# Performance work log

Hardware: AMD Instinct MI355X
Metric: run time of the kernel (lower is better)

The kernel has to match this reference:

```python
import jax, jax.numpy as jnp
import numpy as np

D_MODEL = 768
N_HEAD = 12
D_HEAD = D_MODEL // N_HEAD
B, T = 2, 2048


def setup_inputs() -> dict:
    key = jax.random.key(0)
    k1, k2, k3 = jax.random.split(key, 3)
    x = jax.random.normal(k1, (B, T, D_MODEL), dtype=jnp.float32)
    w_attn = jax.random.normal(k2, (D_MODEL, 3 * D_MODEL), dtype=jnp.float32) * (1.0 / np.sqrt(D_MODEL))
    b_attn = jnp.zeros((3 * D_MODEL,), dtype=jnp.float32)
    w_proj = jax.random.normal(k3, (D_MODEL, D_MODEL), dtype=jnp.float32) * (1.0 / np.sqrt(D_MODEL))
    b_proj = jnp.zeros((D_MODEL,), dtype=jnp.float32)
    return {"x": x, "w_attn": w_attn, "b_attn": b_attn, "w_proj": w_proj, "b_proj": b_proj}


def reference(x, w_attn, b_attn, w_proj, b_proj):
    Bq, Tq, C = x.shape
    qkv = x @ w_attn + b_attn                                  # [B, T, 3C]
    qkv = qkv.reshape(Bq, Tq, 3, N_HEAD, D_HEAD)
    q, k, v = qkv[:, :, 0], qkv[:, :, 1], qkv[:, :, 2]         # [B, T, H, Dh]
    scale = 1.0 / np.sqrt(D_HEAD)
    att = jnp.einsum('bqhd,bkhd->bhqk', q, k) * scale          # [B, H, T, T]
    causal = jnp.tril(jnp.ones((Tq, Tq), dtype=bool))
    att = jnp.where(causal[None, None], att, -jnp.inf)
    att = jax.nn.softmax(att, axis=-1)
    y = jnp.einsum('bhqk,bkhd->bqhd', att, v).reshape(Bq, Tq, C)
    return y @ w_proj + b_proj
```

## Files before the change

### kernel.cpp

```cpp
#include <hip/hip_runtime.h>
#include <hip/hip_bf16.h>

#define D_MODEL 768
#define N_HEADS 12
#define D_HEADK 64
#define BB 2
#define TT 2048
#define M_TOK (BB*TT)
#define N_QKV (3*D_MODEL)
#define MS_SEG (BB*N_HEADS*TT)

using f32x4  = __attribute__((ext_vector_type(4))) float;
using f32x16 = __attribute__((ext_vector_type(16))) float;
using s16x8  = __attribute__((ext_vector_type(8))) short;

typedef __attribute__((address_space(1))) const unsigned int ga_u32;
typedef __attribute__((address_space(3))) unsigned int ls_u32;

__device__ __forceinline__ float fast_exp2(float x) {
    return __builtin_amdgcn_exp2f(x);
}

__device__ __forceinline__ unsigned short f2bf(float f) {
    union { float f; unsigned u; } v; v.f = f;
    unsigned r = v.u + 0x7FFFu + ((v.u >> 16) & 1u);
    return (unsigned short)(r >> 16);
}

__device__ __forceinline__ float bf2f(unsigned short u) {
    union { unsigned u; float f; } v; v.u = ((unsigned)u) << 16; return v.f;
}

__device__ __forceinline__ unsigned cvtpk_bf16(float lo, float hi) {
    unsigned d;
    asm("v_cvt_pk_bf16_f32 %0, %1, %2" : "=v"(d) : "v"(lo), "v"(hi));
    return d;
}

__global__ void xbf_kernel(const float* __restrict__ X, unsigned short* __restrict__ Xb) {
    int idx = (blockIdx.x * 256 + threadIdx.x) * 8;
    float4 v0 = *(const float4*)&X[idx];
    float4 v1 = *(const float4*)&X[idx + 4];
    ushort4 u0, u1;
    u0.x = f2bf(v0.x); u0.y = f2bf(v0.y); u0.z = f2bf(v0.z); u0.w = f2bf(v0.w);
    u1.x = f2bf(v1.x); u1.y = f2bf(v1.y); u1.z = f2bf(v1.z); u1.w = f2bf(v1.w);
    *(ushort4*)&Xb[idx]     = u0;
    *(ushort4*)&Xb[idx + 4] = u1;
}

__global__ void wtrans_kernel(const float* __restrict__ Wa, const float* __restrict__ Wp,
                              unsigned short* __restrict__ Wta, unsigned short* __restrict__ Wtp) {
    const float* W; unsigned short* Wt; int N;
    if (blockIdx.z == 0) { W = Wa; Wt = Wta; N = N_QKV; }
    else                 { W = Wp; Wt = Wtp; N = D_MODEL; }
    int bx = blockIdx.x * 32;
    if (bx >= N) return;
    int by = blockIdx.y * 32;
    __shared__ float tile[32][33];
    int tx = threadIdx.x & 31;
    int ty = threadIdx.x >> 5;
    #pragma unroll
    for (int i = ty; i < 32; i += 8)
        tile[i][tx] = W[(size_t)(by + i) * N + bx + tx];
    __syncthreads();
    #pragma unroll
    for (int i = ty; i < 32; i += 8)
        Wt[(size_t)(bx + i) * D_MODEL + by + tx] = f2bf(tile[tx][i]);
}

__launch_bounds__(256)
__global__ void qkv_kernel(const unsigned short* __restrict__ Xb, const unsigned short* __restrict__ Wt,
                           const float* __restrict__ bias,
                           unsigned short* __restrict__ Qw, unsigned short* __restrict__ Kw,
                           unsigned short* __restrict__ Vw) {
    __shared__ unsigned short As[128*64];
    __shared__ unsigned short Bs[128*64];
    const int m0 = blockIdx.y * 128;
    const int n0 = blockIdx.x * 128;
    const int tid = threadIdx.x;
    const int l  = tid & 63;
    const int w  = tid >> 6;
    const int wr = w >> 1, wc = w & 1;
    const int lr = l & 15, lk4 = l >> 4, li = (l >> 4) * 4;
    const int grw  = l >> 3;
    const int gslt = l & 7;

    f32x4 acc[4][4] = {};
    for (int kt = 0; kt < D_MODEL; kt += 64) {
        #pragma unroll
        for (int i = 0; i < 4; ++i) {
            const int row  = w*32 + i*8 + grw;
            const int gcol = (gslt ^ (row & 7)) << 3;
            __builtin_amdgcn_global_load_lds(
                (ga_u32*)&Xb[(size_t)(m0 + row) * D_MODEL + kt + gcol],
                (ls_u32*)&As[(w*32 + i*8) * 64], 16, 0, 0);
            __builtin_amdgcn_global_load_lds(
                (ga_u32*)&Wt[(size_t)(n0 + row) * D_MODEL + kt + gcol],
                (ls_u32*)&Bs[(w*32 + i*8) * 64], 16, 0, 0);
        }
        __syncthreads();
        #pragma unroll
        for (int ks = 0; ks < 2; ++ks) {
            s16x8 a[4], bf[4];
            #pragma unroll
            for (int mi = 0; mi < 4; ++mi) {
                const int row = wr*64 + mi*16 + lr;
                const int slot = (ks*4 + lk4) ^ (row & 7);
                a[mi] = *(const s16x8*)&As[row*64 + slot*8];
            }
            #pragma unroll
            for (int ni = 0; ni < 4; ++ni) {
                const int row = wc*64 + ni*16 + lr;
                const int slot = (ks*4 + lk4) ^ (row & 7);
                bf[ni] = *(const s16x8*)&Bs[row*64 + slot*8];
            }
            #pragma unroll
            for (int mi = 0; mi < 4; ++mi)
                #pragma unroll
                for (int ni = 0; ni < 4; ++ni)
                    acc[mi][ni] = __builtin_amdgcn_mfma_f32_16x16x32_bf16(a[mi], bf[ni], acc[mi][ni], 0, 0, 0);
        }
        __syncthreads();
    }
    #pragma unroll
    for (int ni = 0; ni < 4; ++ni) {
        int ng = n0 + wc*64 + ni*16 + lr;
        int mat = ng / D_MODEL;
        int hd  = ng % D_MODEL;
        int h = hd >> 6, d = hd & 63;
        float bv = bias[ng];
        #pragma unroll
        for (int mi = 0; mi < 4; ++mi) {
            #pragma unroll
            for (int i = 0; i < 4; ++i) {
                int t  = m0 + wr*64 + mi*16 + li + i;
                int b  = t >> 11, tq = t & 2047;
                float val = acc[mi][ni][i] + bv;
                size_t off = ((size_t)(b*N_HEADS + h)*TT + tq)*64 + d;
                if (mat == 0)      Qw[off] = f2bf(val * 0.18033688f);
                else if (mat == 1) Kw[off] = f2bf(val);
                else               Vw[off] = f2bf(val);
            }
        }
    }
}

__launch_bounds__(256)
__global__ void vtrans_kernel(const unsigned short* __restrict__ Vw, unsigned short* __restrict__ Vt) {
    __shared__ unsigned short tile[64][65];
    const int bh = blockIdx.y;
    const int t0 = blockIdx.x * 64;
    const int tid = threadIdx.x;
    const int srow = tid >> 3;
    const int scol = (tid & 7) * 8;
    const unsigned short* src = Vw + (size_t)bh * TT * 64;
    unsigned short* dst = Vt + (size_t)bh * 64 * TT;
    *(int4*)&tile[srow][scol]    = *(const int4*)&src[(size_t)(t0 + srow) * 64 + scol];
    *(int4*)&tile[srow+32][scol] = *(const int4*)&src[(size_t)(t0 + srow + 32) * 64 + scol];
    __syncthreads();
    s16x8 a0, a1;
    #pragma unroll
    for (int j = 0; j < 8; ++j) {
        a0[j] = (short)tile[scol + j][srow];
        a1[j] = (short)tile[scol + j][srow + 32];
    }
    *(s16x8*)&dst[(size_t)srow * TT + t0 + scol]        = a0;
    *(s16x8*)&dst[(size_t)(srow + 32) * TT + t0 + scol] = a1;
}

__device__ __forceinline__ int swz(int r, int c) { return r*64 + (c ^ ((r & 7) << 3)); }

__launch_bounds__(256)
__global__ void attn_kernel(const unsigned short* __restrict__ Q,
                            const unsigned short* __restrict__ Kk,
                            const unsigned short* __restrict__ Vt,
                            unsigned short* __restrict__ oA,
                            unsigned short* __restrict__ oB,
                            unsigned short* __restrict__ oC,
                            unsigned short* __restrict__ oD,
                            float* __restrict__ ms) {
    __shared__ unsigned short Ks[64*64];
    __shared__ unsigned short Vs[64*64];
    const int bh = blockIdx.y;
    const int px = blockIdx.x;
    const int qci = 15 - (px >> 2);
    const int seg = px & 3;
    const int q0 = qci * 128;
    const int b = bh / N_HEADS, h = bh % N_HEADS;
    const int tid = threadIdx.x;
    const int l  = tid & 63;
    const int w  = tid >> 6;
    const int lq = l & 31;
    const int hi = l >> 5;
    const int srow = tid >> 3;
    const int scol = (tid & 7) * 8;
    const int qw0 = q0 + w * 32;

    const unsigned short* Qp = Q  + (size_t)bh * TT * 64;
    const unsigned short* Kp = Kk + (size_t)bh * TT * 64;
    const unsigned short* Vp = Vt + (size_t)bh * 64 * TT;

    const int ntiles  = 2 * (qci + 1);
    const int t_begin = (seg * ntiles) >> 2;
    const int t_end   = ((seg + 1) * ntiles) >> 2;

    s16x8 qsel[4];
    {
        const unsigned short* qrow = &Qp[(size_t)(qw0 + lq) * 64];
        #pragma unroll
        for (int t = 0; t < 4; ++t) {
            s16x8 qlo = *(const s16x8*)&qrow[16*t];
            s16x8 qhi = *(const s16x8*)&qrow[16*t + 8];
            qsel[t] = hi ? qhi : qlo;
        }
    }

    float mi = -1e30f, si = 0.f;
    f32x16 o0 = {}, o1 = {};

    const int kb0 = t_begin * 64;
    int4 kp0 = *(const int4*)&Kp[(size_t)(kb0 + srow) * 64 + scol];
    int4 kp1 = *(const int4*)&Kp[(size_t)(kb0 + srow + 32) * 64 + scol];
    int4 vp0 = *(const int4*)&Vp[(size_t)srow * TT + kb0 + scol];
    int4 vp1 = *(const int4*)&Vp[(size_t)(srow + 32) * TT + kb0 + scol];

    for (int it = t_begin; it < t_end; ++it) {
        const int kt = it * 64;
        __syncthreads();
        *(int4*)&Ks[swz(srow,      scol)] = kp0;
        *(int4*)&Ks[swz(srow + 32, scol)] = kp1;
        *(int4*)&Vs[swz(srow,      scol)] = vp0;
        *(int4*)&Vs[swz(srow + 32, scol)] = vp1;
        __syncthreads();
        if (it + 1 < t_end) {
            const int k2 = kt + 64;
            kp0 = *(const int4*)&Kp[(size_t)(k2 + srow) * 64 + scol];
            kp1 = *(const int4*)&Kp[(size_t)(k2 + srow + 32) * 64 + scol];
            vp0 = *(const int4*)&Vp[(size_t)srow * TT + k2 + scol];
            vp1 = *(const int4*)&Vp[(size_t)(srow + 32) * TT + k2 + scol];
        }
        #pragma unroll
        for (int kti = 0; kti < 2; ++kti) {
            const int kk = kt + kti * 32;
            if (kk > qw0) continue;
            const bool diag = (kk == qw0);
            f32x16 s = {};
            #pragma unroll
            for (int t = 0; t < 4; ++t) {
                s16x8 a = *(const s16x8*)&Ks[swz(kti*32 + lq, 16*t + 8*hi)];
                s = __builtin_amdgcn_mfma_f32_32x32x16_bf16(a, qsel[t], s, 0, 0, 0);
            }
            if (diag) {
                #pragma unroll
                for (int r = 0; r < 16; ++r) {
                    const int kloc = (r & 3) + 8*(r >> 2) + 4*hi;
                    if (kloc > lq) s[r] = -1e30f;
                }
            }
            float lm = s[0];
            #pragma unroll
            for (int r = 1; r < 16; ++r) lm = fmaxf(lm, s[r]);
            if (!__all(lm <= mi + 11.5f)) {
                float pm = fmaxf(lm, __shfl_xor(lm, 32));
                float mn = fmaxf(mi, pm);
                float sf = fast_exp2(mi - mn);
                si *= sf;
                #pragma unroll
                for (int r = 0; r < 16; ++r) {
                    const int qloc = (r & 3) + 8*(r >> 2) + 4*hi;
                    float sfq = __shfl(sf, qloc);
                    o0[r] *= sfq; o1[r] *= sfq;
                }
                mi = mn;
            }
            float e[16];
            float psum = 0.f;
            #pragma unroll
            for (int r = 0; r < 16; ++r) {
                e[r] = fast_exp2(s[r] - mi);
                psum += e[r];
            }
            si += psum;
            #pragma unroll
            for (int s2 = 0; s2 < 2; ++s2) {
                unsigned c0 = cvtpk_bf16(e[8*s2 + 0], e[8*s2 + 1]);
                unsigned c1 = cvtpk_bf16(e[8*s2 + 2], e[8*s2 + 3]);
                unsigned c2 = cvtpk_bf16(e[8*s2 + 4], e[8*s2 + 5]);
                unsigned c3 = cvtpk_bf16(e[8*s2 + 6], e[8*s2 + 7]);
                asm("v_permlane32_swap_b32 %0, %1" : "+v"(c0), "+v"(c2));
                asm("v_permlane32_swap_b32 %0, %1" : "+v"(c1), "+v"(c3));
                union { unsigned u[4]; s16x8 v; } pa;
                pa.u[0] = c0; pa.u[1] = c1; pa.u[2] = c2; pa.u[3] = c3;
                const int kc = kti*32 + 16*s2 + 8*hi;
                s16x8 vb0 = *(const s16x8*)&Vs[swz(lq,      kc)];
                s16x8 vb1 = *(const s16x8*)&Vs[swz(32 + lq, kc)];
                o0 = __builtin_amdgcn_mfma_f32_32x32x16_bf16(pa.v, vb0, o0, 0, 0, 0);
                o1 = __builtin_amdgcn_mfma_f32_32x32x16_bf16(pa.v, vb1, o1, 0, 0, 0);
            }
        }
    }
    float sfull = si + __shfl_xor(si, 32);
    if (hi == 0) {
        const int row = bh * TT + qw0 + lq;
        ms[seg*MS_SEG + row]       = mi;
        ms[(4+seg)*MS_SEG + row]   = sfull;
    }
    unsigned short* op = (seg == 0) ? oA : (seg == 1) ? oB : (seg == 2) ? oC : oD;
    #pragma unroll
    for (int r = 0; r < 16; ++r) {
        const int qloc = (r & 3) + 8*(r >> 2) + 4*hi;
        size_t row = (size_t)(b*TT + qw0 + qloc) * D_MODEL + h*64;
        op[row + lq]      = f2bf(o0[r]);
        op[row + 32 + lq] = f2bf(o1[r]);
    }
}

__launch_bounds__(256)
__global__ void merge_kernel(const unsigned short* __restrict__ oA,
                             const unsigned short* __restrict__ oB,
                             const unsigned short* __restrict__ oC,
                             const unsigned short* __restrict__ oD,
                             const float* __restrict__ ms,
                             unsigned short* __restrict__ Yw) {
    const int gid = blockIdx.x * 256 + threadIdx.x;
    const int e = gid * 8;
    const int t = e / D_MODEL;
    const int c = e % D_MODEL;
    const int b = t >> 11, q = t & 2047;
    const int h = c >> 6;
    const int row = (b * N_HEADS + h) * TT + q;
    float m0 = ms[row],            m1 = ms[MS_SEG + row];
    float m2 = ms[2*MS_SEG + row], m3 = ms[3*MS_SEG + row];
    float s0 = ms[4*MS_SEG + row], s1 = ms[5*MS_SEG + row];
    float s2 = ms[6*MS_SEG + row], s3 = ms[7*MS_SEG + row];
    float m  = fmaxf(fmaxf(m0, m1), fmaxf(m2, m3));
    float a0 = fast_exp2(m0 - m), a1 = fast_exp2(m1 - m);
    float a2 = fast_exp2(m2 - m), a3 = fast_exp2(m3 - m);
    float inv = 1.f / (s0*a0 + s1*a1 + s2*a2 + s3*a3);
    float w0 = a0*inv, w1 = a1*inv, w2 = a2*inv, w3 = a3*inv;
    s16x8 va = *(const s16x8*)&oA[e];
    s16x8 vb = *(const s16x8*)&oB[e];
    s16x8 vc = *(const s16x8*)&oC[e];
    s16x8 vd = *(const s16x8*)&oD[e];
    s16x8 out;
    #pragma unroll
    for (int j = 0; j < 8; ++j)
        out[j] = (short)f2bf(bf2f((unsigned short)va[j]) * w0 +
                             bf2f((unsigned short)vb[j]) * w1 +
                             bf2f((unsigned short)vc[j]) * w2 +
                             bf2f((unsigned short)vd[j]) * w3);
    *(s16x8*)&Yw[e] = out;
}

__launch_bounds__(256)
__global__ void proj_kernel(const unsigned short* __restrict__ Y, const unsigned short* __restrict__ Wt,
                            const float* __restrict__ bias, float* __restrict__ Out) {
    __shared__ unsigned short As[128][40];
    __shared__ unsigned short Bs[128][40];
    const int m0 = blockIdx.y * 128;
    const int n0 = blockIdx.x * 128;
    const int tid = threadIdx.x;
    const int l  = tid & 63;
    const int w  = tid >> 6;
    const int wr = w >> 1, wc = w & 1;
    const int lr = l & 15, lk = (l >> 4) * 8, li = (l >> 4) * 4;

    f32x4 acc[4][4] = {};
    for (int kt = 0; kt < D_MODEL; kt += 32) {
        #pragma unroll
        for (int p = 0; p < 2; ++p) {
            int ch = tid * 2 + p;
            int r = ch >> 2;
            int c = (ch & 3) * 8;
            *(int4*)&As[r][c] = *(const int4*)&Y[(size_t)(m0 + r) * D_MODEL + kt + c];
            *(int4*)&Bs[r][c] = *(const int4*)&Wt[(size_t)(n0 + r) * D_MODEL + kt + c];
        }
        __syncthreads();
        s16x8 a[4], bf[4];
        #pragma unroll
        for (int mi = 0; mi < 4; ++mi)
            a[mi] = *(const s16x8*)&As[wr*64 + mi*16 + lr][lk];
        #pragma unroll
        for (int ni = 0; ni < 4; ++ni)
            bf[ni] = *(const s16x8*)&Bs[wc*64 + ni*16 + lr][lk];
        #pragma unroll
        for (int mi = 0; mi < 4; ++mi)
            #pragma unroll
            for (int ni = 0; ni < 4; ++ni)
                acc[mi][ni] = __builtin_amdgcn_mfma_f32_16x16x32_bf16(a[mi], bf[ni], acc[mi][ni], 0, 0, 0);
        __syncthreads();
    }
    #pragma unroll
    for (int ni = 0; ni < 4; ++ni) {
        int ng = n0 + wc*64 + ni*16 + lr;
        float bv = bias[ng];
        #pragma unroll
        for (int mj = 0; mj < 4; ++mj)
            #pragma unroll
            for (int i = 0; i < 4; ++i) {
                int t = m0 + wr*64 + mj*16 + li + i;
                Out[(size_t)t*D_MODEL + ng] = acc[mj][ni][i] + bv;
            }
    }
}

extern "C" void kernel_launch(void* const* d_in, const int* in_sizes, int n_in,
                              void* d_out, int out_size, void* d_ws, size_t ws_size,
                              hipStream_t stream) {
    const float* x      = (const float*)d_in[0];
    const float* w_attn = (const float*)d_in[1];
    const float* b_attn = (const float*)d_in[2];
    const float* w_proj = (const float*)d_in[3];
    const float* b_proj = (const float*)d_in[4];
    float* out = (float*)d_out;

    unsigned short* wt_attn = (unsigned short*)d_ws;
    unsigned short* wt_proj = wt_attn + (size_t)N_QKV * D_MODEL;
    unsigned short* Qw      = wt_proj + (size_t)D_MODEL * D_MODEL;
    unsigned short* Kw      = Qw + (size_t)M_TOK * D_MODEL;
    unsigned short* Vw      = Kw + (size_t)M_TOK * D_MODEL;
    unsigned short* Yw      = Vw + (size_t)M_TOK * D_MODEL;
    unsigned short* Xb      = Yw + (size_t)M_TOK * D_MODEL;
    unsigned short* oC      = Xb + (size_t)M_TOK * D_MODEL;
    unsigned short* oD      = oC + (size_t)M_TOK * D_MODEL;
    unsigned short* Vtw     = Xb;
    unsigned short* oA      = Vw;
    unsigned short* oB      = Yw;
    float*          msbuf   = (float*)d_ws;

    hipLaunchKernelGGL(xbf_kernel, dim3(M_TOK*D_MODEL/2048), dim3(256), 0, stream, x, Xb);
    hipLaunchKernelGGL(wtrans_kernel, dim3(N_QKV/32, D_MODEL/32, 2), dim3(256), 0, stream,
                       w_attn, w_proj, wt_attn, wt_proj);
    hipLaunchKernelGGL(qkv_kernel, dim3(N_QKV/128, M_TOK/128), dim3(256), 0, stream,
                       Xb, wt_attn, b_attn, Qw, Kw, Vw);
    hipLaunchKernelGGL(vtrans_kernel, dim3(TT/64, BB*N_HEADS), dim3(256), 0, stream,
                       Vw, Vtw);
    hipLaunchKernelGGL(attn_kernel, dim3(64, BB*N_HEADS), dim3(256), 0, stream,
                       Qw, Kw, Vtw, oA, oB, oC, oD, msbuf);
    hipLaunchKernelGGL(merge_kernel, dim3(M_TOK*D_MODEL/8/256), dim3(256), 0, stream,
                       oA, oB, oC, oD, msbuf, Yw);
    hipLaunchKernelGGL(proj_kernel, dim3(D_MODEL/128, M_TOK/128), dim3(256), 0, stream,
                       Yw, wt_proj, b_proj, out);
}
```

Before: 196.7 us.

## Fuse prep kernels, remap attention blocks to XCDs, add MFMA priority, shrink proj tiles

Merges the x-to-bf16 conversion and the weight transposes into one prep kernel, which saves a launch. Remaps attention block indices so that each XCD handles a fixed group of three heads, aiming for better L2 reuse of K/V. Wraps the attention MFMAs in s_setprio and splits the row-max reduction into a shallower tree. Cuts the projection GEMM tile from 128x128 to 32x128, which raises the block count from 192 to 768 so more CUs are busy, at the cost of more redundant weight loads.

```diff
diff --git a/kernel.cpp b/kernel.cpp
--- a/kernel.cpp
+++ b/kernel.cpp
@@ -37,28 +37,30 @@
     return d;
 }
 
-__global__ void xbf_kernel(const float* __restrict__ X, unsigned short* __restrict__ Xb) {
-    int idx = (blockIdx.x * 256 + threadIdx.x) * 8;
-    float4 v0 = *(const float4*)&X[idx];
-    float4 v1 = *(const float4*)&X[idx + 4];
-    ushort4 u0, u1;
-    u0.x = f2bf(v0.x); u0.y = f2bf(v0.y); u0.z = f2bf(v0.z); u0.w = f2bf(v0.w);
-    u1.x = f2bf(v1.x); u1.y = f2bf(v1.y); u1.z = f2bf(v1.z); u1.w = f2bf(v1.w);
-    *(ushort4*)&Xb[idx]     = u0;
-    *(ushort4*)&Xb[idx + 4] = u1;
-}
-
-__global__ void wtrans_kernel(const float* __restrict__ Wa, const float* __restrict__ Wp,
-                              unsigned short* __restrict__ Wta, unsigned short* __restrict__ Wtp) {
-    const float* W; unsigned short* Wt; int N;
-    if (blockIdx.z == 0) { W = Wa; Wt = Wta; N = N_QKV; }
-    else                 { W = Wp; Wt = Wtp; N = D_MODEL; }
-    int bx = blockIdx.x * 32;
-    if (bx >= N) return;
-    int by = blockIdx.y * 32;
+__global__ void prep_kernel(const float* __restrict__ X, unsigned short* __restrict__ Xb,
+                            const float* __restrict__ Wa, const float* __restrict__ Wp,
+                            unsigned short* __restrict__ Wta, unsigned short* __restrict__ Wtp) {
     __shared__ float tile[32][33];
-    int tx = threadIdx.x & 31;
-    int ty = threadIdx.x >> 5;
+    const int id = blockIdx.x;
+    if (id < 1536) {
+        int idx = (id * 256 + threadIdx.x) * 8;
+        float4 v0 = *(const float4*)&X[idx];
+        float4 v1 = *(const float4*)&X[idx + 4];
+        ushort4 u0, u1;
+        u0.x = f2bf(v0.x); u0.y = f2bf(v0.y); u0.z = f2bf(v0.z); u0.w = f2bf(v0.w);
+        u1.x = f2bf(v1.x); u1.y = f2bf(v1.y); u1.z = f2bf(v1.z); u1.w = f2bf(v1.w);
+        *(ushort4*)&Xb[idx]     = u0;
+        *(ushort4*)&Xb[idx + 4] = u1;
+        return;
+    }
+    const float* W; unsigned short* Wt; int N; int j;
+    if (id < 1536 + 72*24) { j = id - 1536;        W = Wa; Wt = Wta; N = N_QKV; }
+    else                   { j = id - 1536 - 72*24; W = Wp; Wt = Wtp; N = D_MODEL; }
+    const int nb = N / 32;
+    const int bx = (j % nb) * 32;
+    const int by = (j / nb) * 32;
+    const int tx = threadIdx.x & 31;
+    const int ty = threadIdx.x >> 5;
     #pragma unroll
     for (int i = ty; i < 32; i += 8)
         tile[i][tx] = W[(size_t)(by + i) * N + bx + tx];
@@ -181,8 +183,11 @@
                             float* __restrict__ ms) {
     __shared__ unsigned short Ks[64*64];
     __shared__ unsigned short Vs[64*64];
-    const int bh = blockIdx.y;
-    const int px = blockIdx.x;
+    const int f   = blockIdx.y * 64 + blockIdx.x;
+    const int xcd = f & 7;
+    const int rr  = f >> 3;
+    const int bh  = xcd * 3 + (rr % 3);
+    const int px  = rr / 3;
     const int qci = 15 - (px >> 2);
     const int seg = px & 3;
     const int q0 = qci * 128;
@@ -245,11 +250,13 @@
             if (kk > qw0) continue;
             const bool diag = (kk == qw0);
             f32x16 s = {};
+            __builtin_amdgcn_s_setprio(1);
             #pragma unroll
             for (int t = 0; t < 4; ++t) {
                 s16x8 a = *(const s16x8*)&Ks[swz(kti*32 + lq, 16*t + 8*hi)];
                 s = __builtin_amdgcn_mfma_f32_32x32x16_bf16(a, qsel[t], s, 0, 0, 0);
             }
+            __builtin_amdgcn_s_setprio(0);
             if (diag) {
                 #pragma unroll
                 for (int r = 0; r < 16; ++r) {
@@ -257,9 +264,13 @@
                     if (kloc > lq) s[r] = -1e30f;
                 }
             }
-            float lm = s[0];
-            #pragma unroll
-            for (int r = 1; r < 16; ++r) lm = fmaxf(lm, s[r]);
+            float a0m = fmaxf(fmaxf(s[0],  s[1]),  s[2]);
+            float a1m = fmaxf(fmaxf(s[3],  s[4]),  s[5]);
+            float a2m = fmaxf(fmaxf(s[6],  s[7]),  s[8]);
+            float a3m = fmaxf(fmaxf(s[9],  s[10]), s[11]);
+            float a4m = fmaxf(fmaxf(s[12], s[13]), s[14]);
+            float lm  = fmaxf(fmaxf(fmaxf(a0m, a1m), a2m),
+                              fmaxf(fmaxf(a3m, a4m), s[15]));
             if (!__all(lm <= mi + 11.5f)) {
                 float pm = fmaxf(lm, __shfl_xor(lm, 32));
                 float mn = fmaxf(mi, pm);
@@ -294,8 +305,10 @@
                 const int kc = kti*32 + 16*s2 + 8*hi;
                 s16x8 vb0 = *(const s16x8*)&Vs[swz(lq,      kc)];
                 s16x8 vb1 = *(const s16x8*)&Vs[swz(32 + lq, kc)];
+                __builtin_amdgcn_s_setprio(1);
                 o0 = __builtin_amdgcn_mfma_f32_32x32x16_bf16(pa.v, vb0, o0, 0, 0, 0);
                 o1 = __builtin_amdgcn_mfma_f32_32x32x16_bf16(pa.v, vb1, o1, 0, 0, 0);
+                __builtin_amdgcn_s_setprio(0);
             }
         }
     }
@@ -355,51 +368,52 @@
 __launch_bounds__(256)
 __global__ void proj_kernel(const unsigned short* __restrict__ Y, const unsigned short* __restrict__ Wt,
                             const float* __restrict__ bias, float* __restrict__ Out) {
-    __shared__ unsigned short As[128][40];
+    __shared__ unsigned short As[32][40];
     __shared__ unsigned short Bs[128][40];
-    const int m0 = blockIdx.y * 128;
+    const int m0 = blockIdx.y * 32;
     const int n0 = blockIdx.x * 128;
     const int tid = threadIdx.x;
     const int l  = tid & 63;
     const int w  = tid >> 6;
-    const int wr = w >> 1, wc = w & 1;
     const int lr = l & 15, lk = (l >> 4) * 8, li = (l >> 4) * 4;
 
-    f32x4 acc[4][4] = {};
+    f32x4 acc[2][2] = {};
     for (int kt = 0; kt < D_MODEL; kt += 32) {
+        if (tid < 128) {
+            int r = tid >> 2;
+            int c = (tid & 3) * 8;
+            *(int4*)&As[r][c] = *(const int4*)&Y[(size_t)(m0 + r) * D_MODEL + kt + c];
+        }
         #pragma unroll
         for (int p = 0; p < 2; ++p) {
             int ch = tid * 2 + p;
             int r = ch >> 2;
             int c = (ch & 3) * 8;
-            *(int4*)&As[r][c] = *(const int4*)&Y[(size_t)(m0 + r) * D_MODEL + kt + c];
             *(int4*)&Bs[r][c] = *(const int4*)&Wt[(size_t)(n0 + r) * D_MODEL + kt + c];
         }
         __syncthreads();
-        s16x8 a[4], bf[4];
-        #pragma unroll
-        for (int mi = 0; mi < 4; ++mi)
-            a[mi] = *(const s16x8*)&As[wr*64 + mi*16 + lr][lk];
-        #pragma unroll
-        for (int ni = 0; ni < 4; ++ni)
-            bf[ni] = *(const s16x8*)&Bs[wc*64 + ni*16 + lr][lk];
-        #pragma unroll
-        for (int mi = 0; mi < 4; ++mi)
-            #pragma unroll
-            for (int ni = 0; ni < 4; ++ni)
-                acc[mi][ni] = __builtin_amdgcn_mfma_f32_16x16x32_bf16(a[mi], bf[ni], acc[mi][ni], 0, 0, 0);
-        __syncthreads();
-    }
-    #pragma unroll
-    for (int ni = 0; ni < 4; ++ni) {
-        int ng = n0 + wc*64 + ni*16 + lr;
+        s16x8 a[2], bf[2];
+        a[0] = *(const s16x8*)&As[lr][lk];
+        a[1] = *(const s16x8*)&As[16 + lr][lk];
+        bf[0] = *(const s16x8*)&Bs[w*32 + lr][lk];
+        bf[1] = *(const s16x8*)&Bs[w*32 + 16 + lr][lk];
+        #pragma unroll
+        for (int mi2 = 0; mi2 < 2; ++mi2)
+            #pragma unroll
+            for (int ni = 0; ni < 2; ++ni)
+                acc[mi2][ni] = __builtin_amdgcn_mfma_f32_16x16x32_bf16(a[mi2], bf[ni], acc[mi2][ni], 0, 0, 0);
+        __syncthreads();
+    }
+    #pragma unroll
+    for (int ni = 0; ni < 2; ++ni) {
+        int ng = n0 + w*32 + ni*16 + lr;
         float bv = bias[ng];
         #pragma unroll
-        for (int mj = 0; mj < 4; ++mj)
+        for (int mi2 = 0; mi2 < 2; ++mi2)
             #pragma unroll
             for (int i = 0; i < 4; ++i) {
-                int t = m0 + wr*64 + mj*16 + li + i;
-                Out[(size_t)t*D_MODEL + ng] = acc[mj][ni][i] + bv;
+                int t = m0 + mi2*16 + li + i;
+                Out[(size_t)t * D_MODEL + ng] = acc[mi2][ni][i] + bv;
             }
     }
 }
@@ -428,9 +442,8 @@
     unsigned short* oB      = Yw;
     float*          msbuf   = (float*)d_ws;
 
-    hipLaunchKernelGGL(xbf_kernel, dim3(M_TOK*D_MODEL/2048), dim3(256), 0, stream, x, Xb);
-    hipLaunchKernelGGL(wtrans_kernel, dim3(N_QKV/32, D_MODEL/32, 2), dim3(256), 0, stream,
-                       w_attn, w_proj, wt_attn, wt_proj);
+    hipLaunchKernelGGL(prep_kernel, dim3(1536 + 72*24 + 24*24), dim3(256), 0, stream,
+                       x, Xb, w_attn, w_proj, wt_attn, wt_proj);
     hipLaunchKernelGGL(qkv_kernel, dim3(N_QKV/128, M_TOK/128), dim3(256), 0, stream,
                        Xb, wt_attn, b_attn, Qw, Kw, Vw);
     hipLaunchKernelGGL(vtrans_kernel, dim3(TT/64, BB*N_HEADS), dim3(256), 0, stream,
@@ -439,6 +452,6 @@
                        Qw, Kw, Vtw, oA, oB, oC, oD, msbuf);
     hipLaunchKernelGGL(merge_kernel, dim3(M_TOK*D_MODEL/8/256), dim3(256), 0, stream,
                        oA, oB, oC, oD, msbuf, Yw);
-    hipLaunchKernelGGL(proj_kernel, dim3(D_MODEL/128, M_TOK/128), dim3(256), 0, stream,
+    hipLaunchKernelGGL(proj_kernel, dim3(D_MODEL/128, M_TOK/32), dim3(256), 0, stream,
                        Yw, wt_proj, b_proj, out);
 }
```

Measured after the change: 181.4 us. -7.8%, faster.
